# Kernel optimization log

Measured on AMD Instinct MI355X. Metric: run time of the kernel, lower is better.

Reference implementation:

```python
import jax, jax.numpy as jnp
import numpy as np

PAD = 0.1
RESO = 128           # plane_resolution
HID = 128            # hidden_dim
CDIM = 128           # c_dim
NBLK = 5             # n_blocks
PLANES = (('xz', (0, 2)), ('xy', (0, 1)), ('yz', (1, 2)))


def normalize_coordinate(p, dims):
    # p: (B,T,3) -> (B,T,2) in [0, 1)
    xy = p[..., list(dims)] / (1.0 + PAD + 1e-3) + 0.5
    return jnp.clip(xy, 0.0, 1.0 - 1e-5)


def coordinate2index(xy, reso):
    g = (xy * reso).astype(jnp.int32)          # (B,T,2)
    return g[..., 0] + reso * g[..., 1]        # (B,T) flat cell index


def scatter_max_gather(vals, idx, n_cells):
    # vals: (B,T,F), idx: (B,T) -> per-cell max gathered back to points (B,T,F)
    B, T, F = vals.shape
    flat_idx = (idx + jnp.arange(B, dtype=idx.dtype)[:, None] * n_cells).reshape(-1)
    fea = jax.ops.segment_max(vals.reshape(B * T, F), flat_idx, num_segments=B * n_cells)
    return fea[flat_idx].reshape(B, T, F)


def scatter_mean_plane(c, idx, n_cells):
    # c: (B,T,C), idx: (B,T) -> (B, n_cells, C); empty cells stay 0
    B, T, C = c.shape
    flat_idx = (idx + jnp.arange(B, dtype=idx.dtype)[:, None] * n_cells).reshape(-1)
    s = jax.ops.segment_sum(c.reshape(B * T, C), flat_idx, num_segments=B * n_cells)
    cnt = jax.ops.segment_sum(jnp.ones((B * T,), c.dtype), flat_idx, num_segments=B * n_cells)
    return (s / jnp.maximum(cnt, 1.0)[:, None]).reshape(B, n_cells, C)


def resnet_block(x, W0, b0, W1, b1, Ws):
    # ResnetBlockFC(2H -> H), size_h = H, shortcut = Linear(no bias)
    net = jax.nn.relu(x) @ W0 + b0
    dx = jax.nn.relu(net) @ W1 + b1
    return x @ Ws + dx


def setup_inputs() -> dict:
    key = jax.random.key(0)
    ks = jax.random.split(key, 10)
    B, T = 2, 32768
    s = 0.05
    return {
        'p': jax.random.uniform(ks[0], (B, T, 3), jnp.float32, -0.5, 0.5),
        'fc_pos_W': s * jax.random.normal(ks[1], (3, 2 * HID), jnp.float32),
        'fc_pos_b': s * jax.random.normal(ks[2], (2 * HID,), jnp.float32),
        'blocks_W0': s * jax.random.normal(ks[3], (NBLK, 2 * HID, HID), jnp.float32),
        'blocks_b0': s * jax.random.normal(ks[4], (NBLK, HID), jnp.float32),
        'blocks_W1': s * jax.random.normal(ks[5], (NBLK, HID, HID), jnp.float32),
        'blocks_b1': s * jax.random.normal(ks[6], (NBLK, HID), jnp.float32),
        'blocks_Ws': s * jax.random.normal(ks[7], (NBLK, 2 * HID, HID), jnp.float32),
        'fc_c_W': s * jax.random.normal(ks[8], (HID, CDIM), jnp.float32),
        'fc_c_b': s * jax.random.normal(ks[9], (CDIM,), jnp.float32),
    }


def reference(p, fc_pos_W, fc_pos_b, blocks_W0, blocks_b0, blocks_W1, blocks_b1,
              blocks_Ws, fc_c_W, fc_c_b):
    B, T, _ = p.shape
    R2 = RESO * RESO
    index = {k: coordinate2index(normalize_coordinate(p, d), RESO) for k, d in PLANES}

    net = p @ fc_pos_W + fc_pos_b                       # (B,T,2H)
    net = resnet_block(net, blocks_W0[0], blocks_b0[0],
                       blocks_W1[0], blocks_b1[0], blocks_Ws[0])  # (B,T,H)
    for i in range(1, NBLK):
        pooled = sum(scatter_max_gather(net, index[k], R2) for k, _ in PLANES)
        net = jnp.concatenate([net, pooled], axis=-1)   # (B,T,2H)
        net = resnet_block(net, blocks_W0[i], blocks_b0[i],
                           blocks_W1[i], blocks_b1[i], blocks_Ws[i])

    c = net @ fc_c_W + fc_c_b                           # (B,T,C)
    planes = []
    for k, _ in PLANES:  # order: xz, xy, yz
        fea = scatter_mean_plane(c, index[k], R2)       # (B,R2,C)
        planes.append(fea.transpose(0, 2, 1).reshape(B, CDIM, RESO, RESO))
    return jnp.stack(planes)                            # (3,B,C,R,R)
```

## Files before the change

kernel.cpp:

```cpp
#include <hip/hip_runtime.h>

#define TT 65536
#define R2 16384

typedef _Float16 f16x8 __attribute__((ext_vector_type(8)));
typedef float    f32x4 __attribute__((ext_vector_type(4)));
typedef unsigned u32x4 __attribute__((ext_vector_type(4)));

#define MFMA16 __builtin_amdgcn_mfma_f32_16x16x32_f16

__device__ __forceinline__ unsigned short f2h(float f){
    _Float16 h = (_Float16)f;
    return __builtin_bit_cast(unsigned short, h);
}
__device__ __forceinline__ float h2f(unsigned short u){
    return (float)__builtin_bit_cast(_Float16, u);
}
__device__ __forceinline__ unsigned relu2(unsigned w){
    unsigned s = w & 0x80008000u;
    unsigned mask = ((s >> 15) * 0x7FFFu) | s;
    return w & ~mask;
}
__device__ __forceinline__ float nrm(float a){
    float v = a / 1.101f + 0.5f;
    v = fmaxf(v, 0.0f);
    v = fminf(v, 0.99999f);
    return v;
}

__global__ __launch_bounds__(256) void k_repack(const float* __restrict__ W0,
        const float* __restrict__ W1, const float* __restrict__ Ws,
        const float* __restrict__ Wc, unsigned short* __restrict__ out){
    int e = blockIdx.x*256 + threadIdx.x;
    const float* src; int r;
    if (e < 409600){
        int i = e / 81920; r = e % 81920;
        if (r < 32768)      { src = W0 + (size_t)i*32768; }
        else if (r < 49152) { src = W1 + (size_t)i*16384; r -= 32768; }
        else                { src = Ws + (size_t)i*32768; r -= 49152; }
    } else { src = Wc; r = e - 409600; }
    int j = r & 7, l = (r >> 3) & 63, t = (r >> 9) & 7, ks = r >> 12;
    int k = ks*32 + (l >> 4)*8 + j;
    int n = t*16 + (l & 15);
    out[e] = f2h(src[k*128 + n]);
}

__global__ __launch_bounds__(256) void k_idxhist(const float* __restrict__ p,
        int* __restrict__ idx, int* __restrict__ cnt){
    int pt = blockIdx.x*256 + threadIdx.x;
    float p0 = p[pt*3+0], p1 = p[pt*3+1], p2 = p[pt*3+2];
    int g0 = (int)(nrm(p0)*128.f);
    int g1 = (int)(nrm(p1)*128.f);
    int g2 = (int)(nrm(p2)*128.f);
    int i0 = g0 + 128*g2, i1 = g0 + 128*g1, i2 = g1 + 128*g2;
    idx[0*TT + pt] = i0;
    idx[1*TT + pt] = i1;
    idx[2*TT + pt] = i2;
    int b14 = (pt >> 15) << 14;
    atomicAdd(&cnt[0*32768 + b14 + i0], 1);
    atomicAdd(&cnt[1*32768 + b14 + i1], 1);
    atomicAdd(&cnt[2*32768 + b14 + i2], 1);
}

__global__ __launch_bounds__(1024) void k_scan(const int* __restrict__ cnt,
        int* __restrict__ cs, int* __restrict__ cp){
    __shared__ int ls[1024];
    int pl = blockIdx.x, tid = threadIdx.x;
    const int* c = cnt + pl*32768;
    int v[32], tot = 0;
    #pragma unroll
    for (int j = 0; j < 32; j++){ v[j] = c[tid*32 + j]; tot += v[j]; }
    int x = tot;
    ls[tid] = x; __syncthreads();
    for (int off = 1; off < 1024; off <<= 1){
        int add = (tid >= off) ? ls[tid - off] : 0;
        __syncthreads();
        x += add; ls[tid] = x;
        __syncthreads();
    }
    int run = x - tot;
    #pragma unroll
    for (int j = 0; j < 32; j++){
        cs[pl*32769 + tid*32 + j] = run;
        cp[pl*32768 + tid*32 + j] = run;
        run += v[j];
    }
    if (tid == 1023) cs[pl*32769 + 32768] = TT;
}

__global__ __launch_bounds__(256) void k_scatter(const int* __restrict__ idx,
        int* __restrict__ cp, int* __restrict__ srt){
    int pt = blockIdx.x*256 + threadIdx.x;
    int b14 = (pt >> 15) << 14;
    #pragma unroll
    for (int pl = 0; pl < 3; pl++){
        int pos = atomicAdd(&cp[pl*32768 + b14 + idx[pl*TT + pt]], 1);
        srt[pl*TT + pos] = pt;
    }
}

__global__ __launch_bounds__(256) void k_pool3(const unsigned short* __restrict__ xb,
        const int* __restrict__ srt, const int* __restrict__ cs,
        unsigned short* __restrict__ mxp){
    int pl = blockIdx.y;
    const int* srtp = srt + (size_t)pl*TT;
    const int* csp  = cs  + (size_t)pl*32769;
    int lane = threadIdx.x & 63;
    int c = blockIdx.x*4 + (threadIdx.x >> 6);
    int s = csp[c], e = csp[c+1];
    if (s == e) return;
    float m0 = -1e30f, m1 = -1e30f;
    int pt = srtp[s];
    for (int i = s; i < e; i++){
        int ptn = (i+1 < e) ? srtp[i+1] : 0;
        unsigned v = ((const unsigned*)(xb + (size_t)pt*256))[lane];
        m0 = fmaxf(m0, h2f((unsigned short)(v & 0xFFFF)));
        m1 = fmaxf(m1, h2f((unsigned short)(v >> 16)));
        pt = ptn;
    }
    unsigned pk = (unsigned)f2h(m0) | ((unsigned)f2h(m1) << 16);
    ((unsigned*)(mxp + ((size_t)pl*32768 + c)*128))[lane] = pk;
}

__global__ __launch_bounds__(256, 2) void k_resnet(unsigned short* __restrict__ xb,
        const unsigned short* __restrict__ wp,
        const float* __restrict__ b0, const float* __restrict__ b1,
        const int* __restrict__ idx, const unsigned short* __restrict__ mxp,
        const float* __restrict__ pin, const float* __restrict__ fW,
        const float* __restrict__ fb,
        const unsigned short* __restrict__ wc, const float* __restrict__ bc){
    __shared__ __align__(16) unsigned short lds[32768];
    unsigned short* lw = lds;
    unsigned short* lt = lds + 16384;
    int tid = threadIdx.x, w = tid >> 6, lane = tid & 63;
    int quad = lane >> 4, l15 = lane & 15;
    int m0 = blockIdx.x*128 + w*32;
    float b0v[8], b1v[8];
    #pragma unroll
    for (int t = 0; t < 8; t++){ b0v[t] = b0[t*16 + l15]; b1v[t] = b1[t*16 + l15]; }

    u32x4 pre[8];
    auto preload = [&](const unsigned short* src){
        const u32x4* g = (const u32x4*)src;
        #pragma unroll
        for (int i = 0; i < 8; i++) pre[i] = g[i*256 + tid];
    };
    auto flush = [&](){
        u32x4* l = (u32x4*)lw;
        #pragma unroll
        for (int i = 0; i < 8; i++) l[i*256 + tid] = pre[i];
    };

    preload(wp);

    u32x4 xf[2][4]; f16x8 pf[2][4];
    if (pin){
        #pragma unroll
        for (int s = 0; s < 2; s++){
            int row = m0 + s*16 + l15;
            float p0 = pin[row*3+0], p1 = pin[row*3+1], p2 = pin[row*3+2];
            #pragma unroll
            for (int ks = 0; ks < 4; ks++){
                int c0 = ks*32 + quad*8;
                unsigned short hx[8], hp[8];
                #pragma unroll
                for (int h = 0; h < 2; h++){
                    f32x4 w0 = *(const f32x4*)(fW + c0 + h*4);
                    f32x4 w1 = *(const f32x4*)(fW + 256 + c0 + h*4);
                    f32x4 w2 = *(const f32x4*)(fW + 512 + c0 + h*4);
                    f32x4 bb = *(const f32x4*)(fb + c0 + h*4);
                    f32x4 v0 = *(const f32x4*)(fW + 128 + c0 + h*4);
                    f32x4 v1 = *(const f32x4*)(fW + 384 + c0 + h*4);
                    f32x4 v2 = *(const f32x4*)(fW + 640 + c0 + h*4);
                    f32x4 bp = *(const f32x4*)(fb + 128 + c0 + h*4);
                    #pragma unroll
                    for (int j = 0; j < 4; j++){
                        hx[h*4+j] = f2h(bb[j] + p0*w0[j] + p1*w1[j] + p2*w2[j]);
                        hp[h*4+j] = f2h(bp[j] + p0*v0[j] + p1*v1[j] + p2*v2[j]);
                    }
                }
                unsigned short* dx = (unsigned short*)&xf[s][ks];
                unsigned short* dp = (unsigned short*)&pf[s][ks];
                #pragma unroll
                for (int j = 0; j < 8; j++){ dx[j] = hx[j]; dp[j] = hp[j]; }
            }
        }
    } else {
        #pragma unroll
        for (int s = 0; s < 2; s++){
            size_t rb = (size_t)(m0 + s*16 + l15)*256;
            #pragma unroll
            for (int ks = 0; ks < 4; ks++)
                xf[s][ks] = *(const u32x4*)(xb + rb + ks*32 + quad*8);
        }
        #pragma unroll
        for (int s = 0; s < 2; s++){
            int row = m0 + s*16 + l15;
            int b14 = (row >> 15) << 14;
            const unsigned short* q0 = mxp + ((size_t)(0*32768 + b14 + idx[row]))*128;
            const unsigned short* q1 = mxp + ((size_t)(1*32768 + b14 + idx[TT + row]))*128;
            const unsigned short* q2 = mxp + ((size_t)(2*32768 + b14 + idx[2*TT + row]))*128;
            #pragma unroll
            for (int ks = 0; ks < 4; ks++){
                int col = ks*32 + quad*8;
                f16x8 a = *(const f16x8*)(q0 + col);
                f16x8 b = *(const f16x8*)(q1 + col);
                f16x8 c = *(const f16x8*)(q2 + col);
                f16x8 r;
                #pragma unroll
                for (int j = 0; j < 8; j++)
                    r[j] = (_Float16)((float)a[j] + (float)b[j] + (float)c[j]);
                pf[s][ks] = r;
            }
        }
    }

    f32x4 acc[2][8];
    #pragma unroll
    for (int s = 0; s < 2; s++)
        #pragma unroll
        for (int t = 0; t < 8; t++){ f32x4 z = {0.f,0.f,0.f,0.f}; acc[s][t] = z; }

    __syncthreads(); flush(); __syncthreads();
    preload(wp + 16384);
    {
        #pragma unroll
        for (int ks = 0; ks < 4; ks++){
            u32x4 u0 = xf[0][ks], u1 = xf[1][ks];
            u0.x = relu2(u0.x); u0.y = relu2(u0.y); u0.z = relu2(u0.z); u0.w = relu2(u0.w);
            u1.x = relu2(u1.x); u1.y = relu2(u1.y); u1.z = relu2(u1.z); u1.w = relu2(u1.w);
            f16x8 a0 = __builtin_bit_cast(f16x8, u0);
            f16x8 a1 = __builtin_bit_cast(f16x8, u1);
            #pragma unroll
            for (int t = 0; t < 8; t++){
                f16x8 b = *(const f16x8*)&lw[((ks*8 + t)*64 + lane)*8];
                acc[0][t] = MFMA16(a0, b, acc[0][t], 0, 0, 0);
                acc[1][t] = MFMA16(a1, b, acc[1][t], 0, 0, 0);
            }
        }
    }

    __syncthreads(); flush(); __syncthreads();
    preload(wp + 32768);
    {
        #pragma unroll
        for (int ks = 0; ks < 4; ks++){
            u32x4 u0 = __builtin_bit_cast(u32x4, pf[0][ks]);
            u32x4 u1 = __builtin_bit_cast(u32x4, pf[1][ks]);
            u0.x = relu2(u0.x); u0.y = relu2(u0.y); u0.z = relu2(u0.z); u0.w = relu2(u0.w);
            u1.x = relu2(u1.x); u1.y = relu2(u1.y); u1.z = relu2(u1.z); u1.w = relu2(u1.w);
            f16x8 a0 = __builtin_bit_cast(f16x8, u0);
            f16x8 a1 = __builtin_bit_cast(f16x8, u1);
            #pragma unroll
            for (int t = 0; t < 8; t++){
                f16x8 b = *(const f16x8*)&lw[((ks*8 + t)*64 + lane)*8];
                acc[0][t] = MFMA16(a0, b, acc[0][t], 0, 0, 0);
                acc[1][t] = MFMA16(a1, b, acc[1][t], 0, 0, 0);
            }
        }
    }

    __syncthreads(); flush(); __syncthreads();
    preload(wp + 49152);
    f32x4 acc2[2][8];
    #pragma unroll
    for (int s = 0; s < 2; s++){
        int strip = w*2 + s;
        #pragma unroll
        for (int t = 0; t < 8; t++){
            int ks2 = t >> 1;
            int l2b = ((t & 1)*2 + ((lane >> 3) & 1))*16 + quad*4;
            #pragma unroll
            for (int r = 0; r < 4; r++){
                float v = acc[s][t][r] + b0v[t];
                v = fmaxf(v, 0.f);
                lt[(((ks2*8 + strip)*64) + l2b + r)*8 + (lane & 7)] = f2h(v);
            }
        }
    }
    #pragma unroll
    for (int s = 0; s < 2; s++)
        #pragma unroll
        for (int t = 0; t < 8; t++){ f32x4 iv = {b1v[t],b1v[t],b1v[t],b1v[t]}; acc2[s][t] = iv; }
    #pragma unroll
    for (int ks = 0; ks < 4; ks++){
        f16x8 a0 = *(const f16x8*)&lt[((ks*8 + w*2 + 0)*64 + lane)*8];
        f16x8 a1 = *(const f16x8*)&lt[((ks*8 + w*2 + 1)*64 + lane)*8];
        #pragma unroll
        for (int t = 0; t < 8; t++){
            f16x8 b = *(const f16x8*)&lw[((ks*8 + t)*64 + lane)*8];
            acc2[0][t] = MFMA16(a0, b, acc2[0][t], 0, 0, 0);
            acc2[1][t] = MFMA16(a1, b, acc2[1][t], 0, 0, 0);
        }
    }

    __syncthreads(); flush(); __syncthreads();
    preload(wp + 65536);
    {
        #pragma unroll
        for (int ks = 0; ks < 4; ks++){
            f16x8 a0 = __builtin_bit_cast(f16x8, xf[0][ks]);
            f16x8 a1 = __builtin_bit_cast(f16x8, xf[1][ks]);
            #pragma unroll
            for (int t = 0; t < 8; t++){
                f16x8 b = *(const f16x8*)&lw[((ks*8 + t)*64 + lane)*8];
                acc2[0][t] = MFMA16(a0, b, acc2[0][t], 0, 0, 0);
                acc2[1][t] = MFMA16(a1, b, acc2[1][t], 0, 0, 0);
            }
        }
    }

    __syncthreads(); flush(); __syncthreads();
    if (wc) preload(wc);
    {
        #pragma unroll
        for (int ks = 0; ks < 4; ks++){
            f16x8 a0 = pf[0][ks];
            f16x8 a1 = pf[1][ks];
            #pragma unroll
            for (int t = 0; t < 8; t++){
                f16x8 b = *(const f16x8*)&lw[((ks*8 + t)*64 + lane)*8];
                acc2[0][t] = MFMA16(a0, b, acc2[0][t], 0, 0, 0);
                acc2[1][t] = MFMA16(a1, b, acc2[1][t], 0, 0, 0);
            }
        }
    }

    if (!wc){
        #pragma unroll
        for (int s = 0; s < 2; s++)
            #pragma unroll
            for (int t = 0; t < 8; t++)
                #pragma unroll
                for (int r = 0; r < 4; r++){
                    int row = m0 + s*16 + quad*4 + r;
                    xb[(size_t)row*256 + t*16 + l15] = f2h(acc2[s][t][r]);
                }
        return;
    }

    __syncthreads(); flush(); __syncthreads();
    #pragma unroll
    for (int s = 0; s < 2; s++){
        int strip = w*2 + s;
        #pragma unroll
        for (int t = 0; t < 8; t++){
            int ks2 = t >> 1;
            int l2b = ((t & 1)*2 + ((lane >> 3) & 1))*16 + quad*4;
            #pragma unroll
            for (int r = 0; r < 4; r++)
                lt[(((ks2*8 + strip)*64) + l2b + r)*8 + (lane & 7)] = f2h(acc2[s][t][r]);
        }
    }
    f32x4 acc3[2][8];
    #pragma unroll
    for (int t = 0; t < 8; t++){
        float bv = bc[t*16 + l15];
        f32x4 iv = {bv, bv, bv, bv};
        acc3[0][t] = iv; acc3[1][t] = iv;
    }
    #pragma unroll
    for (int ks = 0; ks < 4; ks++){
        f16x8 a0 = *(const f16x8*)&lt[((ks*8 + w*2 + 0)*64 + lane)*8];
        f16x8 a1 = *(const f16x8*)&lt[((ks*8 + w*2 + 1)*64 + lane)*8];
        #pragma unroll
        for (int t = 0; t < 8; t++){
            f16x8 b = *(const f16x8*)&lw[((ks*8 + t)*64 + lane)*8];
            acc3[0][t] = MFMA16(a0, b, acc3[0][t], 0, 0, 0);
            acc3[1][t] = MFMA16(a1, b, acc3[1][t], 0, 0, 0);
        }
    }
    #pragma unroll
    for (int s = 0; s < 2; s++)
        #pragma unroll
        for (int t = 0; t < 8; t++)
            #pragma unroll
            for (int r = 0; r < 4; r++){
                int row = m0 + s*16 + quad*4 + r;
                xb[(size_t)row*256 + 128 + t*16 + l15] = f2h(acc3[s][t][r]);
            }
}

__global__ __launch_bounds__(1024) void k_psum3(const unsigned short* __restrict__ xb,
        const int* __restrict__ srt, const int* __restrict__ cs,
        float* __restrict__ out){
    __shared__ float ls[32*129];
    int pl = blockIdx.y;
    const int* srtp = srt + (size_t)pl*TT;
    const int* csp  = cs  + (size_t)pl*32769;
    int w = threadIdx.x >> 6, lane = threadIdx.x & 63;
    int c0 = blockIdx.x * 32;
    #pragma unroll
    for (int cc = w; cc < 32; cc += 16){
        int c = c0 + cc;
        int s = csp[c], e = csp[c+1];
        float s0 = 0.f, s1 = 0.f;
        if (s < e){
            int pt = srtp[s];
            for (int i = s; i < e; i++){
                int ptn = (i+1 < e) ? srtp[i+1] : 0;
                unsigned v = ((const unsigned*)(xb + (size_t)pt*256 + 128))[lane];
                s0 += h2f((unsigned short)(v & 0xFFFF));
                s1 += h2f((unsigned short)(v >> 16));
                pt = ptn;
            }
        }
        float rc = (e > s) ? 1.f/(float)(e - s) : 0.f;
        ls[cc*129 + lane*2]     = s0*rc;
        ls[cc*129 + lane*2 + 1] = s1*rc;
    }
    __syncthreads();
    int pb = pl*2 + (c0 >> 14);
    float* o = out + (size_t)pb*128*R2 + (c0 & 16383);
    #pragma unroll
    for (int j = 0; j < 4; j++){
        int lin = j*1024 + threadIdx.x;
        int f = lin >> 5, cc = lin & 31;
        o[(size_t)f*R2 + cc] = ls[cc*129 + f];
    }
}

extern "C" void kernel_launch(void* const* d_in, const int* in_sizes, int n_in,
                              void* d_out, int out_size, void* d_ws, size_t ws_size,
                              hipStream_t stream) {
    const float* p        = (const float*)d_in[0];
    const float* fc_pos_W = (const float*)d_in[1];
    const float* fc_pos_b = (const float*)d_in[2];
    const float* bW0      = (const float*)d_in[3];
    const float* bb0      = (const float*)d_in[4];
    const float* bW1      = (const float*)d_in[5];
    const float* bb1      = (const float*)d_in[6];
    const float* bWs      = (const float*)d_in[7];
    const float* fc_c_W   = (const float*)d_in[8];
    const float* fc_c_b   = (const float*)d_in[9];
    float* out = (float*)d_out;

    char* ws = (char*)d_ws;
    int*            idx   = (int*)ws;
    unsigned short* xbuf  = (unsigned short*)(ws + 786432);
    int*            srt   = (int*)(ws + 34340864);
    int*            cs    = (int*)(ws + 35127296);
    int*            cp    = (int*)(ws + 35520528);
    unsigned short* wpack = (unsigned short*)(ws + 35913744);
    unsigned short* mxp   = (unsigned short*)(ws + 36765712);

    k_repack<<<1664, 256, 0, stream>>>(bW0, bW1, bWs, fc_c_W, wpack);
    hipMemsetAsync(cp, 0, (size_t)3*32768*4, stream);
    k_idxhist<<<TT/256, 256, 0, stream>>>(p, idx, cp);
    k_scan   <<<3, 1024, 0, stream>>>(cp, cs, cp);
    k_scatter<<<TT/256, 256, 0, stream>>>(idx, cp, srt);

    k_resnet<<<512, 256, 0, stream>>>(xbuf, wpack, bb0, bb1,
            idx, (const unsigned short*)nullptr,
            p, fc_pos_W, fc_pos_b,
            (const unsigned short*)nullptr, (const float*)nullptr);

    for (int i = 1; i < 5; i++){
        k_pool3<<<dim3(8192, 3), 256, 0, stream>>>(xbuf, srt, cs, mxp);
        const unsigned short* wc = (i == 4) ? (wpack + 409600) : (const unsigned short*)nullptr;
        const float* bcp = (i == 4) ? fc_c_b : (const float*)nullptr;
        k_resnet<<<512, 256, 0, stream>>>(xbuf, wpack + (size_t)i*81920,
                bb0 + (size_t)i*128, bb1 + (size_t)i*128,
                idx, mxp,
                (const float*)nullptr, (const float*)nullptr, (const float*)nullptr,
                wc, bcp);
    }

    k_psum3<<<dim3(1024, 3), 1024, 0, stream>>>(xbuf, srt, cs, out);
}
```

Baseline: 412.8 us.

## Stream resnet weights from global into register double buffers instead of staging in LDS

Each wave now loads its MFMA B-operand fragments for the next k-slice straight from global memory into one of two register buffers while computing on the other. This replaces the cooperative preload/flush of whole weight matrices into LDS and the paired __syncthreads around each stage. The aim is to drop block-wide barriers, halve the LDS footprint, and overlap weight fetches with MFMA work. In exchange, each of the four waves re-reads the same weights, which relies on L1/L2 hits and raises register pressure.

```diff
diff --git a/kernel.cpp b/kernel.cpp
--- a/kernel.cpp
+++ b/kernel.cpp
@@ -122,6 +122,39 @@
     ((unsigned*)(mxp + ((size_t)pl*32768 + c)*128))[lane] = pk;
 }
 
+#define SEG(ACC, CURB, NEXTB, GETA)                                   \
+  { _Pragma("unroll")                                                 \
+    for (int ks = 0; ks < 4; ks++){                                   \
+      f16x8* cur = (ks & 1) ? bq1 : bq0;                              \
+      f16x8* nxt = (ks & 1) ? bq0 : bq1;                              \
+      const unsigned short* nb = (ks < 3) ? (CURB) : (NEXTB);         \
+      int nks = (ks < 3) ? ks + 1 : 0;                                \
+      if (nb) ld8(nxt, nb, nks);                                      \
+      f16x8 a0, a1;                                                   \
+      GETA                                                            \
+      _Pragma("unroll")                                               \
+      for (int t = 0; t < 8; t++){                                    \
+        ACC[0][t] = MFMA16(a0, cur[t], ACC[0][t], 0, 0, 0);           \
+        ACC[1][t] = MFMA16(a1, cur[t], ACC[1][t], 0, 0, 0);           \
+      }                                                               \
+    }                                                                 \
+  }
+
+#define A_RELU_XF { u32x4 u0 = xf[0][ks], u1 = xf[1][ks];                         \
+    u0.x=relu2(u0.x); u0.y=relu2(u0.y); u0.z=relu2(u0.z); u0.w=relu2(u0.w);       \
+    u1.x=relu2(u1.x); u1.y=relu2(u1.y); u1.z=relu2(u1.z); u1.w=relu2(u1.w);       \
+    a0 = __builtin_bit_cast(f16x8, u0); a1 = __builtin_bit_cast(f16x8, u1); }
+#define A_RELU_PF { u32x4 u0 = __builtin_bit_cast(u32x4, pf[0][ks]);              \
+    u32x4 u1 = __builtin_bit_cast(u32x4, pf[1][ks]);                              \
+    u0.x=relu2(u0.x); u0.y=relu2(u0.y); u0.z=relu2(u0.z); u0.w=relu2(u0.w);       \
+    u1.x=relu2(u1.x); u1.y=relu2(u1.y); u1.z=relu2(u1.z); u1.w=relu2(u1.w);       \
+    a0 = __builtin_bit_cast(f16x8, u0); a1 = __builtin_bit_cast(f16x8, u1); }
+#define A_XF { a0 = __builtin_bit_cast(f16x8, xf[0][ks]);                         \
+               a1 = __builtin_bit_cast(f16x8, xf[1][ks]); }
+#define A_PF { a0 = pf[0][ks]; a1 = pf[1][ks]; }
+#define A_LT { a0 = *(const f16x8*)&lt[((ks*8 + w*2 + 0)*64 + lane)*8];           \
+               a1 = *(const f16x8*)&lt[((ks*8 + w*2 + 1)*64 + lane)*8]; }
+
 __global__ __launch_bounds__(256, 2) void k_resnet(unsigned short* __restrict__ xb,
         const unsigned short* __restrict__ wp,
         const float* __restrict__ b0, const float* __restrict__ b1,
@@ -129,9 +162,7 @@
         const float* __restrict__ pin, const float* __restrict__ fW,
         const float* __restrict__ fb,
         const unsigned short* __restrict__ wc, const float* __restrict__ bc){
-    __shared__ __align__(16) unsigned short lds[32768];
-    unsigned short* lw = lds;
-    unsigned short* lt = lds + 16384;
+    __shared__ __align__(16) unsigned short lt[16384];
     int tid = threadIdx.x, w = tid >> 6, lane = tid & 63;
     int quad = lane >> 4, l15 = lane & 15;
     int m0 = blockIdx.x*128 + w*32;
@@ -139,19 +170,14 @@
     #pragma unroll
     for (int t = 0; t < 8; t++){ b0v[t] = b0[t*16 + l15]; b1v[t] = b1[t*16 + l15]; }
 
-    u32x4 pre[8];
-    auto preload = [&](const unsigned short* src){
-        const u32x4* g = (const u32x4*)src;
-        #pragma unroll
-        for (int i = 0; i < 8; i++) pre[i] = g[i*256 + tid];
+    f16x8 bq0[8], bq1[8];
+    auto ld8 = [&](f16x8* dst, const unsigned short* base, int ks){
+        #pragma unroll
+        for (int t = 0; t < 8; t++)
+            dst[t] = *(const f16x8*)(base + ((size_t)((ks*8 + t)*64 + lane))*8);
     };
-    auto flush = [&](){
-        u32x4* l = (u32x4*)lw;
-        #pragma unroll
-        for (int i = 0; i < 8; i++) l[i*256 + tid] = pre[i];
-    };
-
-    preload(wp);
+
+    ld8(bq0, wp, 0);
 
     u32x4 xf[2][4]; f16x8 pf[2][4];
     if (pin){
@@ -221,48 +247,9 @@
         #pragma unroll
         for (int t = 0; t < 8; t++){ f32x4 z = {0.f,0.f,0.f,0.f}; acc[s][t] = z; }
 
-    __syncthreads(); flush(); __syncthreads();
-    preload(wp + 16384);
-    {
-        #pragma unroll
-        for (int ks = 0; ks < 4; ks++){
-            u32x4 u0 = xf[0][ks], u1 = xf[1][ks];
-            u0.x = relu2(u0.x); u0.y = relu2(u0.y); u0.z = relu2(u0.z); u0.w = relu2(u0.w);
-            u1.x = relu2(u1.x); u1.y = relu2(u1.y); u1.z = relu2(u1.z); u1.w = relu2(u1.w);
-            f16x8 a0 = __builtin_bit_cast(f16x8, u0);
-            f16x8 a1 = __builtin_bit_cast(f16x8, u1);
-            #pragma unroll
-            for (int t = 0; t < 8; t++){
-                f16x8 b = *(const f16x8*)&lw[((ks*8 + t)*64 + lane)*8];
-                acc[0][t] = MFMA16(a0, b, acc[0][t], 0, 0, 0);
-                acc[1][t] = MFMA16(a1, b, acc[1][t], 0, 0, 0);
-            }
-        }
-    }
-
-    __syncthreads(); flush(); __syncthreads();
-    preload(wp + 32768);
-    {
-        #pragma unroll
-        for (int ks = 0; ks < 4; ks++){
-            u32x4 u0 = __builtin_bit_cast(u32x4, pf[0][ks]);
-            u32x4 u1 = __builtin_bit_cast(u32x4, pf[1][ks]);
-            u0.x = relu2(u0.x); u0.y = relu2(u0.y); u0.z = relu2(u0.z); u0.w = relu2(u0.w);
-            u1.x = relu2(u1.x); u1.y = relu2(u1.y); u1.z = relu2(u1.z); u1.w = relu2(u1.w);
-            f16x8 a0 = __builtin_bit_cast(f16x8, u0);
-            f16x8 a1 = __builtin_bit_cast(f16x8, u1);
-            #pragma unroll
-            for (int t = 0; t < 8; t++){
-                f16x8 b = *(const f16x8*)&lw[((ks*8 + t)*64 + lane)*8];
-                acc[0][t] = MFMA16(a0, b, acc[0][t], 0, 0, 0);
-                acc[1][t] = MFMA16(a1, b, acc[1][t], 0, 0, 0);
-            }
-        }
-    }
-
-    __syncthreads(); flush(); __syncthreads();
-    preload(wp + 49152);
-    f32x4 acc2[2][8];
+    SEG(acc, wp,         wp + 16384, A_RELU_XF)
+    SEG(acc, wp + 16384, wp + 32768, A_RELU_PF)
+
     #pragma unroll
     for (int s = 0; s < 2; s++){
         int strip = w*2 + s;
@@ -278,53 +265,16 @@
             }
         }
     }
+
+    f32x4 acc2[2][8];
     #pragma unroll
     for (int s = 0; s < 2; s++)
         #pragma unroll
         for (int t = 0; t < 8; t++){ f32x4 iv = {b1v[t],b1v[t],b1v[t],b1v[t]}; acc2[s][t] = iv; }
-    #pragma unroll
-    for (int ks = 0; ks < 4; ks++){
-        f16x8 a0 = *(const f16x8*)&lt[((ks*8 + w*2 + 0)*64 + lane)*8];
-        f16x8 a1 = *(const f16x8*)&lt[((ks*8 + w*2 + 1)*64 + lane)*8];
-        #pragma unroll
-        for (int t = 0; t < 8; t++){
-            f16x8 b = *(const f16x8*)&lw[((ks*8 + t)*64 + lane)*8];
-            acc2[0][t] = MFMA16(a0, b, acc2[0][t], 0, 0, 0);
-            acc2[1][t] = MFMA16(a1, b, acc2[1][t], 0, 0, 0);
-        }
-    }
-
-    __syncthreads(); flush(); __syncthreads();
-    preload(wp + 65536);
-    {
-        #pragma unroll
-        for (int ks = 0; ks < 4; ks++){
-            f16x8 a0 = __builtin_bit_cast(f16x8, xf[0][ks]);
-            f16x8 a1 = __builtin_bit_cast(f16x8, xf[1][ks]);
-            #pragma unroll
-            for (int t = 0; t < 8; t++){
-                f16x8 b = *(const f16x8*)&lw[((ks*8 + t)*64 + lane)*8];
-                acc2[0][t] = MFMA16(a0, b, acc2[0][t], 0, 0, 0);
-                acc2[1][t] = MFMA16(a1, b, acc2[1][t], 0, 0, 0);
-            }
-        }
-    }
-
-    __syncthreads(); flush(); __syncthreads();
-    if (wc) preload(wc);
-    {
-        #pragma unroll
-        for (int ks = 0; ks < 4; ks++){
-            f16x8 a0 = pf[0][ks];
-            f16x8 a1 = pf[1][ks];
-            #pragma unroll
-            for (int t = 0; t < 8; t++){
-                f16x8 b = *(const f16x8*)&lw[((ks*8 + t)*64 + lane)*8];
-                acc2[0][t] = MFMA16(a0, b, acc2[0][t], 0, 0, 0);
-                acc2[1][t] = MFMA16(a1, b, acc2[1][t], 0, 0, 0);
-            }
-        }
-    }
+    SEG(acc2, wp + 32768, wp + 49152, A_LT)
+
+    SEG(acc2, wp + 49152, wp + 65536, A_XF)
+    SEG(acc2, wp + 65536, wc,         A_PF)
 
     if (!wc){
         #pragma unroll
@@ -339,7 +289,6 @@
         return;
     }
 
-    __syncthreads(); flush(); __syncthreads();
     #pragma unroll
     for (int s = 0; s < 2; s++){
         int strip = w*2 + s;
@@ -359,17 +308,7 @@
         f32x4 iv = {bv, bv, bv, bv};
         acc3[0][t] = iv; acc3[1][t] = iv;
     }
-    #pragma unroll
-    for (int ks = 0; ks < 4; ks++){
-        f16x8 a0 = *(const f16x8*)&lt[((ks*8 + w*2 + 0)*64 + lane)*8];
-        f16x8 a1 = *(const f16x8*)&lt[((ks*8 + w*2 + 1)*64 + lane)*8];
-        #pragma unroll
-        for (int t = 0; t < 8; t++){
-            f16x8 b = *(const f16x8*)&lw[((ks*8 + t)*64 + lane)*8];
-            acc3[0][t] = MFMA16(a0, b, acc3[0][t], 0, 0, 0);
-            acc3[1][t] = MFMA16(a1, b, acc3[1][t], 0, 0, 0);
-        }
-    }
+    SEG(acc3, wc, (const unsigned short*)nullptr, A_LT)
     #pragma unroll
     for (int s = 0; s < 2; s++)
         #pragma unroll
```

Result: slower. 423.7 us (+2.6%).
